# Kernel optimization log

Measured on AMD Instinct MI355X. Metric: run time of the kernel, lower is better.

Reference implementation:

```python
import jax, jax.numpy as jnp
import numpy as np

B, H, S, D = 2, 16, 2048, 128


def setup_inputs() -> dict:
    key = jax.random.key(0)
    kq, kk, kv = jax.random.split(key, 3)
    q1 = jax.random.normal(kq, (B, H, S, D), dtype=jnp.float32)
    k1 = jax.random.normal(kk, (B, H, S, D), dtype=jnp.float32)
    v1 = jax.random.normal(kv, (B, H, S, D), dtype=jnp.float32)
    scale_factor = jnp.float32(1.0 / np.sqrt(D))
    dropout_p = jnp.float32(0.5)
    return {"q1": q1, "k1": k1, "v1": v1, "scale_factor": scale_factor, "dropout_p": dropout_p}


def reference(q1, k1, v1, scale_factor, dropout_p):
    # scores: [B,H,S,S]
    qk = jnp.einsum("bhqd,bhkd->bhqk", q1, k1)
    softmax_qk = jax.nn.softmax(qk * scale_factor, axis=-1)
    # dropout (training mode, as in F.dropout default): keep w.p. 1-p, scale by 1/(1-p)
    keep = jax.random.bernoulli(jax.random.key(42), 1.0 - dropout_p, softmax_qk.shape)
    dropout_qk = jnp.where(keep, softmax_qk / (1.0 - dropout_p), 0.0)
    # output: [B,H,S,D]
    return jnp.einsum("bhqk,bhkd->bhqd", dropout_qk, v1)
```

## Files before the change

### kernel.cpp

```cpp
#include <hip/hip_runtime.h>

typedef float    f32x4  __attribute__((ext_vector_type(4)));
typedef __bf16   bf16x8 __attribute__((ext_vector_type(8)));
typedef unsigned int u32;
typedef unsigned int u32x4 __attribute__((ext_vector_type(4)));
typedef unsigned short u16;

#define S_LEN 2048
#define D_DIM 128
#define NHEAD 32
#define QBLK  64
#define KVBLK 64
#define WS_NEED (2u * NHEAD * S_LEN * D_DIM * 2u)

__device__ __forceinline__ u32 rotl32(u32 x, int r) {
  return __builtin_amdgcn_alignbit(x, x, 32 - r);
}

__device__ __forceinline__ u32 threefry_bits(u32 ctr) {
  const u32 ks1 = 42u;
  const u32 ks2 = 0x1BD11BF0u;
  u32 x0 = 0u;
  u32 x1 = ctr + ks1;
#define TFR(r) { x0 += x1; x1 = rotl32(x1, (r)); x1 ^= x0; }
  TFR(13) TFR(15) TFR(26) TFR(6)
  x0 += ks1; x1 += ks2 + 1u;
  TFR(17) TFR(29) TFR(16) TFR(24)
  x0 += ks2; x1 += 2u;
  TFR(13) TFR(15) TFR(26) TFR(6)
  x1 += ks1 + 3u;
  TFR(17) TFR(29) TFR(16) TFR(24)
  x0 += ks1; x1 += ks2 + 4u;
  TFR(13) TFR(15) TFR(26) TFR(6)
  x0 += ks2; x1 += 5u;
#undef TFR
  return x0 ^ x1;
}

__device__ __forceinline__ u16 f2bf(float f) {
  u32 u = __float_as_uint(f);
  return (u16)((u + 0x7fffu + ((u >> 16) & 1u)) >> 16);
}

__device__ __forceinline__ u32 cvtpk(float lo, float hi) {
  u32 r;
  asm("v_cvt_pk_bf16_f32 %0, %1, %2" : "=v"(r) : "v"(lo), "v"(hi));
  return r;
}

__device__ __forceinline__ float exp2a(float x) {
  float r;
  asm("v_exp_f32 %0, %1" : "=v"(r) : "v"(x));
  return r;
}

__device__ __forceinline__ void gl_lds16(const void* g, void* l) {
  __builtin_amdgcn_global_load_lds(
      (const __attribute__((address_space(1))) void*)g,
      (__attribute__((address_space(3))) void*)l, 16, 0, 0);
}

__device__ __forceinline__ u32 swzv(int d) { return (u32)((d & 7) ^ ((d >> 2) & 7)); }

__global__ void __launch_bounds__(256) prepack(
    const float* __restrict__ Kp, const float* __restrict__ Vp,
    u16* __restrict__ kimg, u16* __restrict__ vimg)
{
  __shared__ u16 vt[KVBLK * D_DIM];
  const int blk = blockIdx.x;
  const int h = blk >> 5, tk = blk & 31;
  const float* Kh = Kp + ((size_t)h * S_LEN + (size_t)tk * KVBLK) * D_DIM;
  const float* Vh = Vp + ((size_t)h * S_LEN + (size_t)tk * KVBLK) * D_DIM;
  u16* kd = kimg + (size_t)blk * (KVBLK * D_DIM);
  u16* vd = vimg + (size_t)blk * (KVBLK * D_DIM);
  const int t = threadIdx.x;

#pragma unroll
  for (int it = 0; it < 4; ++it) {
    u32 p = (u32)(it * 256 + t) * 16;
    u32 krow = p >> 8;
    u32 cb = (p & 255) ^ ((krow & 7) << 4);
    const float* src = Kh + krow * D_DIM + (cb >> 1);
    f32x4 a = *(const f32x4*)(src);
    f32x4 b = *(const f32x4*)(src + 4);
    u32x4 o;
    o.x = cvtpk(a[0], a[1]); o.y = cvtpk(a[2], a[3]);
    o.z = cvtpk(b[0], b[1]); o.w = cvtpk(b[2], b[3]);
    *(u32x4*)((char*)kd + p) = o;
  }
#pragma unroll
  for (int it = 0; it < 8; ++it) {
    int g = it * 256 + t;
    int kv = g >> 5, d4 = g & 31;
    f32x4 x = *(const f32x4*)(Vh + (size_t)kv * D_DIM + d4 * 4);
    u32* dst = (u32*)(vt + kv * D_DIM + d4 * 4);
    dst[0] = cvtpk(x[0], x[1]);
    dst[1] = cvtpk(x[2], x[3]);
  }
  __syncthreads();
#pragma unroll
  for (int it = 0; it < 4; ++it) {
    u32 p = (u32)(it * 256 + t) * 16;
    u32 vdr = p >> 7;
    u32 cb = (p & 127) ^ (swzv((int)vdr) << 4);
    u32 kv0 = cb >> 1;
    u16 e[8];
#pragma unroll
    for (int i = 0; i < 8; ++i) e[i] = vt[(kv0 + i) * D_DIM + vdr];
    u32x4 o;
    o.x = (u32)e[0] | ((u32)e[1] << 16);
    o.y = (u32)e[2] | ((u32)e[3] << 16);
    o.z = (u32)e[4] | ((u32)e[5] << 16);
    o.w = (u32)e[6] | ((u32)e[7] << 16);
    *(u32x4*)((char*)vd + p) = o;
  }
}

__global__ void __launch_bounds__(256) attn_fwd(
    const float* __restrict__ Qp, const u16* __restrict__ kimg,
    const u16* __restrict__ vimg, const float* __restrict__ scp,
    const float* __restrict__ dpp, float* __restrict__ Op)
{
  __shared__ alignas(16) u16 kbuf[KVBLK * D_DIM];
  __shared__ alignas(16) u16 vbuf[D_DIM * KVBLK];
  __shared__ alignas(16) u16 pbuf[4][16 * KVBLK];

  const int n    = blockIdx.y * gridDim.x + blockIdx.x;
  const int head = ((n & 7) << 2) | ((n >> 3) & 3);
  const int qblk = n >> 5;
  const int t  = threadIdx.x;
  const int w  = t >> 6;
  const int l  = t & 63;
  const int lg = l >> 4;
  const int lc = l & 15;

  const float scale  = scp[0];
  const float keep_p = 1.0f - dpp[0];
  const float qmul   = scale * 1.44269504088896340736f;

  u32 ithr;
  {
    float T = keep_p * 8388608.0f;
    u32 Ti = (u32)T;
    u32 thr9 = ((float)Ti == T) ? Ti : (Ti + 1u);
    ithr = (thr9 >= (1u << 23)) ? 0xFFFFFFFFu : (thr9 << 9);
  }

  const float* __restrict__ Qh = Qp + (size_t)head * (S_LEN * D_DIM);
  float*       __restrict__ Oh = Op + (size_t)head * (S_LEN * D_DIM);

  bf16x8 qf[4];
  {
    const int qrow = qblk * QBLK + w * 16 + lc;
    const float* qsrc = Qh + (size_t)qrow * D_DIM + lg * 8;
#pragma unroll
    for (int kc = 0; kc < 4; ++kc) {
      f32x4 a = *(const f32x4*)(qsrc + kc * 32);
      f32x4 b = *(const f32x4*)(qsrc + kc * 32 + 4);
      union { u32 w4[4]; bf16x8 v; } uu;
      uu.w4[0] = cvtpk(a[0] * qmul, a[1] * qmul);
      uu.w4[1] = cvtpk(a[2] * qmul, a[3] * qmul);
      uu.w4[2] = cvtpk(b[0] * qmul, b[1] * qmul);
      uu.w4[3] = cvtpk(b[2] * qmul, b[3] * qmul);
      qf[kc] = uu.v;
    }
  }

  f32x4 acc[8];
#pragma unroll
  for (int dt = 0; dt < 8; ++dt) acc[dt] = f32x4{0.f, 0.f, 0.f, 0.f};
  float lrun[4] = { 0.f, 0.f, 0.f, 0.f };

  u16* pb = &pbuf[w][0];
  const u32 qrow_c0 = (u32)(qblk * QBLK + w * 16 + lg * 4);
  const u32 ibase0  = ((u32)head * S_LEN + qrow_c0) * S_LEN;

  for (int tkv = 0; tkv < S_LEN / KVBLK; ++tkv) {
    const u16* kt  = kimg + (size_t)(head * 32 + tkv) * (KVBLK * D_DIM);
    const u16* vtg = vimg + (size_t)(head * 32 + tkv) * (KVBLK * D_DIM);
#pragma unroll
    for (int it = 0; it < 4; ++it) {
      int ck = it * 4 + w;
      gl_lds16((const char*)kt  + ck * 1024 + l * 16, (char*)kbuf + ck * 1024);
      gl_lds16((const char*)vtg + ck * 1024 + l * 16, (char*)vbuf + ck * 1024);
    }
    __syncthreads();

    f32x4 sa[4];
#pragma unroll
    for (int ct = 0; ct < 4; ++ct) sa[ct] = f32x4{0.f, 0.f, 0.f, 0.f};
#pragma unroll
    for (int kc = 0; kc < 4; ++kc) {
#pragma unroll
      for (int ct = 0; ct < 4; ++ct) {
        int krow = ct * 16 + lc;
        u32 koff = ((u32)(krow * 256 + (lg * 8 + kc * 32) * 2)) ^ ((u32)(krow & 7) << 4);
        bf16x8 kf = *(const bf16x8*)((char*)kbuf + koff);
        sa[ct] = __builtin_amdgcn_mfma_f32_16x16x32_bf16(qf[kc], kf, sa[ct], 0, 0, 0);
      }
    }

#pragma unroll
    for (int j = 0; j < 4; ++j) {
      u32 ib = ibase0 + (u32)j * S_LEN + (u32)(tkv * KVBLK) + (u32)lc;
      float p0 = exp2a(sa[0][j]);
      float p1 = exp2a(sa[1][j]);
      float p2 = exp2a(sa[2][j]);
      float p3 = exp2a(sa[3][j]);
      lrun[j] += (p0 + p1) + (p2 + p3);
      u32 b0 = threefry_bits(ib);
      u32 b1 = threefry_bits(ib + 16u);
      u32 b2 = threefry_bits(ib + 32u);
      u32 b3 = threefry_bits(ib + 48u);
      float m0 = (b0 < ithr) ? p0 : 0.0f;
      float m1 = (b1 < ithr) ? p1 : 0.0f;
      float m2 = (b2 < ithr) ? p2 : 0.0f;
      float m3 = (b3 < ithr) ? p3 : 0.0f;
      u32 pk01 = cvtpk(m0, m1);
      u32 pk23 = cvtpk(m2, m3);
      int prow = lg * 4 + j;
      u32 rb = (u32)(prow * 128 + lc * 2);
      u32 sw = (u32)(prow & 7) << 4;
      *(u16*)((char*)pb + ((rb      ) ^ sw)) = (u16)pk01;
      *(u16*)((char*)pb + ((rb +  32) ^ sw)) = (u16)(pk01 >> 16);
      *(u16*)((char*)pb + ((rb +  64) ^ sw)) = (u16)pk23;
      *(u16*)((char*)pb + ((rb +  96) ^ sw)) = (u16)(pk23 >> 16);
    }

#pragma unroll
    for (int kc2 = 0; kc2 < 2; ++kc2) {
      u32 poff = ((u32)(lc * 128 + (lg * 8 + kc2 * 32) * 2)) ^ ((u32)(lc & 7) << 4);
      bf16x8 pa = *(const bf16x8*)((char*)pb + poff);
#pragma unroll
      for (int dt = 0; dt < 8; ++dt) {
        int vd = dt * 16 + lc;
        u32 voff = ((u32)(vd * 128 + (lg * 8 + kc2 * 32) * 2)) ^ (swzv(vd) << 4);
        bf16x8 vb = *(const bf16x8*)((char*)vbuf + voff);
        acc[dt] = __builtin_amdgcn_mfma_f32_16x16x32_bf16(pa, vb, acc[dt], 0, 0, 0);
      }
    }
    __syncthreads();
  }

#pragma unroll
  for (int j = 0; j < 4; ++j) {
    float ls = lrun[j];
    ls += __shfl_xor(ls, 1, 64);
    ls += __shfl_xor(ls, 2, 64);
    ls += __shfl_xor(ls, 4, 64);
    ls += __shfl_xor(ls, 8, 64);
    float sc = (1.0f / keep_p) / ls;
    u32 qg = qrow_c0 + (u32)j;
#pragma unroll
    for (int dt = 0; dt < 8; ++dt) {
      Oh[(size_t)qg * D_DIM + dt * 16 + lc] = acc[dt][j] * sc;
    }
  }
}

__global__ void __launch_bounds__(256) attn_fwd_fb(
    const float* __restrict__ Qp, const float* __restrict__ Kp,
    const float* __restrict__ Vp, const float* __restrict__ scp,
    const float* __restrict__ dpp, float* __restrict__ Op)
{
  __shared__ alignas(16) u16 kbuf[KVBLK * D_DIM];
  __shared__ alignas(16) u16 vbuf[D_DIM * KVBLK];
  __shared__ alignas(16) u16 pbuf[4][16 * KVBLK];

  const int n    = blockIdx.y * gridDim.x + blockIdx.x;
  const int head = ((n & 7) << 2) | ((n >> 3) & 3);
  const int qblk = n >> 5;
  const int t  = threadIdx.x;
  const int w  = t >> 6;
  const int l  = t & 63;
  const int lg = l >> 4;
  const int lc = l & 15;

  const float scale  = scp[0];
  const float keep_p = 1.0f - dpp[0];
  const float qmul   = scale * 1.44269504088896340736f;
  u32 ithr;
  {
    float T = keep_p * 8388608.0f;
    u32 Ti = (u32)T;
    u32 thr9 = ((float)Ti == T) ? Ti : (Ti + 1u);
    ithr = (thr9 >= (1u << 23)) ? 0xFFFFFFFFu : (thr9 << 9);
  }

  const float* __restrict__ Qh = Qp + (size_t)head * (S_LEN * D_DIM);
  const float* __restrict__ Kh = Kp + (size_t)head * (S_LEN * D_DIM);
  const float* __restrict__ Vh = Vp + (size_t)head * (S_LEN * D_DIM);
  float*       __restrict__ Oh = Op + (size_t)head * (S_LEN * D_DIM);

  bf16x8 qf[4];
  {
    const int qrow = qblk * QBLK + w * 16 + lc;
    const float* qsrc = Qh + (size_t)qrow * D_DIM + lg * 8;
#pragma unroll
    for (int kc = 0; kc < 4; ++kc) {
      f32x4 a = *(const f32x4*)(qsrc + kc * 32);
      f32x4 b = *(const f32x4*)(qsrc + kc * 32 + 4);
      union { u16 h[8]; bf16x8 v; } uu;
#pragma unroll
      for (int i = 0; i < 4; ++i) {
        uu.h[i]     = f2bf(a[i] * qmul);
        uu.h[4 + i] = f2bf(b[i] * qmul);
      }
      qf[kc] = uu.v;
    }
  }

  f32x4 acc[8];
#pragma unroll
  for (int dt = 0; dt < 8; ++dt) acc[dt] = f32x4{0.f, 0.f, 0.f, 0.f};
  float lrun[4] = { 0.f, 0.f, 0.f, 0.f };

  u16* pb = &pbuf[w][0];
  const u32 qrow_c0 = (u32)(qblk * QBLK + w * 16 + lg * 4);
  const u32 ibase0  = ((u32)head * S_LEN + qrow_c0) * S_LEN;

  for (int tkv = 0; tkv < S_LEN / KVBLK; ++tkv) {
#pragma unroll
    for (int r = 0; r < 8; ++r) {
      int g = r * 256 + t;
      int kv = g >> 5, d4 = g & 31;
      f32x4 x = *(const f32x4*)(Kh + (size_t)(tkv * KVBLK + kv) * D_DIM + d4 * 4);
      u32 w0 = (u32)f2bf(x[0]) | ((u32)f2bf(x[1]) << 16);
      u32 w1 = (u32)f2bf(x[2]) | ((u32)f2bf(x[3]) << 16);
      u32 off = ((u32)(kv * 256 + d4 * 8)) ^ ((u32)(kv & 7) << 4);
      u32* dst = (u32*)((char*)kbuf + off);
      dst[0] = w0; dst[1] = w1;
    }
#pragma unroll
    for (int r = 0; r < 8; ++r) {
      int rowloc = w * 16 + (r & 1) * 8 + (l >> 3);
      int d4     = (r >> 1) * 8 + (l & 7);
      f32x4 x = *(const f32x4*)(Vh + (size_t)(tkv * KVBLK + rowloc) * D_DIM + d4 * 4);
      u16 mb0 = f2bf(x[0]), mb1 = f2bf(x[1]), mb2 = f2bf(x[2]), mb3 = f2bf(x[3]);
      u16 pb0 = (u16)__shfl_xor((int)mb0, 8, 64);
      u16 pb1 = (u16)__shfl_xor((int)mb1, 8, 64);
      u16 pb2 = (u16)__shfl_xor((int)mb2, 8, 64);
      u16 pb3 = (u16)__shfl_xor((int)mb3, 8, 64);
      bool ev = ((l >> 3) & 1) == 0;
      int kvp = rowloc & ~1;
      u32 wA = ev ? ((u32)mb0 | ((u32)pb0 << 16)) : ((u32)pb2 | ((u32)mb2 << 16));
      u32 wB = ev ? ((u32)mb1 | ((u32)pb1 << 16)) : ((u32)pb3 | ((u32)mb3 << 16));
      int dA = d4 * 4 + (ev ? 0 : 2);
      u32 offA = ((u32)(dA * 128 + kvp * 2)) ^ (swzv(dA) << 4);
      u32 offB = ((u32)((dA + 1) * 128 + kvp * 2)) ^ (swzv(dA + 1) << 4);
      *(u32*)((char*)vbuf + offA) = wA;
      *(u32*)((char*)vbuf + offB) = wB;
    }
    __syncthreads();

    f32x4 sa[4];
#pragma unroll
    for (int ct = 0; ct < 4; ++ct) sa[ct] = f32x4{0.f, 0.f, 0.f, 0.f};
#pragma unroll
    for (int kc = 0; kc < 4; ++kc) {
#pragma unroll
      for (int ct = 0; ct < 4; ++ct) {
        int krow = ct * 16 + lc;
        u32 koff = ((u32)(krow * 256 + (lg * 8 + kc * 32) * 2)) ^ ((u32)(krow & 7) << 4);
        bf16x8 kf = *(const bf16x8*)((char*)kbuf + koff);
        sa[ct] = __builtin_amdgcn_mfma_f32_16x16x32_bf16(qf[kc], kf, sa[ct], 0, 0, 0);
      }
    }

#pragma unroll
    for (int j = 0; j < 4; ++j) {
      u32 ib = ibase0 + (u32)j * S_LEN + (u32)(tkv * KVBLK) + (u32)lc;
      float p0 = exp2a(sa[0][j]);
      float p1 = exp2a(sa[1][j]);
      float p2 = exp2a(sa[2][j]);
      float p3 = exp2a(sa[3][j]);
      lrun[j] += (p0 + p1) + (p2 + p3);
      u32 b0 = threefry_bits(ib);
      u32 b1 = threefry_bits(ib + 16u);
      u32 b2 = threefry_bits(ib + 32u);
      u32 b3 = threefry_bits(ib + 48u);
      float m0 = (b0 < ithr) ? p0 : 0.0f;
      float m1 = (b1 < ithr) ? p1 : 0.0f;
      float m2 = (b2 < ithr) ? p2 : 0.0f;
      float m3 = (b3 < ithr) ? p3 : 0.0f;
      u32 pk01 = cvtpk(m0, m1);
      u32 pk23 = cvtpk(m2, m3);
      int prow = lg * 4 + j;
      u32 rb = (u32)(prow * 128 + lc * 2);
      u32 sw = (u32)(prow & 7) << 4;
      *(u16*)((char*)pb + ((rb      ) ^ sw)) = (u16)pk01;
      *(u16*)((char*)pb + ((rb +  32) ^ sw)) = (u16)(pk01 >> 16);
      *(u16*)((char*)pb + ((rb +  64) ^ sw)) = (u16)pk23;
      *(u16*)((char*)pb + ((rb +  96) ^ sw)) = (u16)(pk23 >> 16);
    }

#pragma unroll
    for (int kc2 = 0; kc2 < 2; ++kc2) {
      u32 poff = ((u32)(lc * 128 + (lg * 8 + kc2 * 32) * 2)) ^ ((u32)(lc & 7) << 4);
      bf16x8 pa = *(const bf16x8*)((char*)pb + poff);
#pragma unroll
      for (int dt = 0; dt < 8; ++dt) {
        int vd = dt * 16 + lc;
        u32 voff = ((u32)(vd * 128 + (lg * 8 + kc2 * 32) * 2)) ^ (swzv(vd) << 4);
        bf16x8 vb = *(const bf16x8*)((char*)vbuf + voff);
        acc[dt] = __builtin_amdgcn_mfma_f32_16x16x32_bf16(pa, vb, acc[dt], 0, 0, 0);
      }
    }
    __syncthreads();
  }

#pragma unroll
  for (int j = 0; j < 4; ++j) {
    float ls = lrun[j];
    ls += __shfl_xor(ls, 1, 64);
    ls += __shfl_xor(ls, 2, 64);
    ls += __shfl_xor(ls, 4, 64);
    ls += __shfl_xor(ls, 8, 64);
    float sc = (1.0f / keep_p) / ls;
    u32 qg = qrow_c0 + (u32)j;
#pragma unroll
    for (int dt = 0; dt < 8; ++dt) {
      Oh[(size_t)qg * D_DIM + dt * 16 + lc] = acc[dt][j] * sc;
    }
  }
}

extern "C" void kernel_launch(void* const* d_in, const int* in_sizes, int n_in,
                              void* d_out, int out_size, void* d_ws, size_t ws_size,
                              hipStream_t stream) {
  const float* q  = (const float*)d_in[0];
  const float* k  = (const float*)d_in[1];
  const float* v  = (const float*)d_in[2];
  const float* sc = (const float*)d_in[3];
  const float* dp = (const float*)d_in[4];
  float* out = (float*)d_out;
  dim3 grid(S_LEN / QBLK, NHEAD);
  dim3 block(256);
  if (ws_size >= (size_t)WS_NEED) {
    u16* kimg = (u16*)d_ws;
    u16* vimg = kimg + (size_t)NHEAD * S_LEN * D_DIM;
    hipLaunchKernelGGL(prepack, dim3(NHEAD * (S_LEN / KVBLK)), dim3(256), 0, stream, k, v, kimg, vimg);
    hipLaunchKernelGGL(attn_fwd, grid, block, 0, stream, q, kimg, vimg, sc, dp, out);
  } else {
    hipLaunchKernelGGL(attn_fwd_fb, grid, block, 0, stream, q, k, v, sc, dp, out);
  }
}
```

Measured before the change: 323.3 us.

## Grow query tile to 128 rows with 8 waves sharing each K/V tile

The main attention kernel now processes 128 query rows per block using 8 waves (512 threads) instead of 64 rows with 4 waves. Each K/V tile staged into shared memory is shared by twice as many waves, which halves the per-block global-to-LDS load traffic per query row. The grid is flattened to one dimension and the fallback kernel keeps its 64-row tiling. The trade-off is fewer, larger blocks (512 blocks) and more per-block LDS for the P buffers, which may lower occupancy or leave some tail imbalance.

```diff
diff --git a/kernel.cpp b/kernel.cpp
--- a/kernel.cpp
+++ b/kernel.cpp
@@ -9,8 +9,9 @@
 #define S_LEN 2048
 #define D_DIM 128
 #define NHEAD 32
-#define QBLK  64
+#define QBLK  128
 #define KVBLK 64
+#define NWAVE 8
 #define WS_NEED (2u * NHEAD * S_LEN * D_DIM * 2u)
 
 __device__ __forceinline__ u32 rotl32(u32 x, int r) {
@@ -116,16 +117,16 @@
   }
 }
 
-__global__ void __launch_bounds__(256) attn_fwd(
+__global__ void __launch_bounds__(512, 4) attn_fwd(
     const float* __restrict__ Qp, const u16* __restrict__ kimg,
     const u16* __restrict__ vimg, const float* __restrict__ scp,
     const float* __restrict__ dpp, float* __restrict__ Op)
 {
   __shared__ alignas(16) u16 kbuf[KVBLK * D_DIM];
   __shared__ alignas(16) u16 vbuf[D_DIM * KVBLK];
-  __shared__ alignas(16) u16 pbuf[4][16 * KVBLK];
-
-  const int n    = blockIdx.y * gridDim.x + blockIdx.x;
+  __shared__ alignas(16) u16 pbuf[NWAVE][16 * KVBLK];
+
+  const int n    = blockIdx.x;
   const int head = ((n & 7) << 2) | ((n >> 3) & 3);
   const int qblk = n >> 5;
   const int t  = threadIdx.x;
@@ -148,6 +149,8 @@
 
   const float* __restrict__ Qh = Qp + (size_t)head * (S_LEN * D_DIM);
   float*       __restrict__ Oh = Op + (size_t)head * (S_LEN * D_DIM);
+  const u16* __restrict__ kim = kimg + (size_t)head * 32 * (KVBLK * D_DIM);
+  const u16* __restrict__ vim = vimg + (size_t)head * 32 * (KVBLK * D_DIM);
 
   bf16x8 qf[4];
   {
@@ -176,13 +179,15 @@
   const u32 ibase0  = ((u32)head * S_LEN + qrow_c0) * S_LEN;
 
   for (int tkv = 0; tkv < S_LEN / KVBLK; ++tkv) {
-    const u16* kt  = kimg + (size_t)(head * 32 + tkv) * (KVBLK * D_DIM);
-    const u16* vtg = vimg + (size_t)(head * 32 + tkv) * (KVBLK * D_DIM);
-#pragma unroll
-    for (int it = 0; it < 4; ++it) {
-      int ck = it * 4 + w;
-      gl_lds16((const char*)kt  + ck * 1024 + l * 16, (char*)kbuf + ck * 1024);
-      gl_lds16((const char*)vtg + ck * 1024 + l * 16, (char*)vbuf + ck * 1024);
+    {
+      const u16* kt_ = kim + (size_t)tkv * (KVBLK * D_DIM);
+      const u16* vt_ = vim + (size_t)tkv * (KVBLK * D_DIM);
+#pragma unroll
+      for (int it = 0; it < 2; ++it) {
+        int ck = it * 8 + w;
+        gl_lds16((const char*)kt_ + ck * 1024 + l * 16, (char*)kbuf + ck * 1024);
+        gl_lds16((const char*)vt_ + ck * 1024 + l * 16, (char*)vbuf + ck * 1024);
+      }
     }
     __syncthreads();
 
@@ -294,7 +299,7 @@
 
   bf16x8 qf[4];
   {
-    const int qrow = qblk * QBLK + w * 16 + lc;
+    const int qrow = qblk * 64 + w * 16 + lc;
     const float* qsrc = Qh + (size_t)qrow * D_DIM + lg * 8;
 #pragma unroll
     for (int kc = 0; kc < 4; ++kc) {
@@ -316,7 +321,7 @@
   float lrun[4] = { 0.f, 0.f, 0.f, 0.f };
 
   u16* pb = &pbuf[w][0];
-  const u32 qrow_c0 = (u32)(qblk * QBLK + w * 16 + lg * 4);
+  const u32 qrow_c0 = (u32)(qblk * 64 + w * 16 + lg * 4);
   const u32 ibase0  = ((u32)head * S_LEN + qrow_c0) * S_LEN;
 
   for (int tkv = 0; tkv < S_LEN / KVBLK; ++tkv) {
@@ -434,14 +439,13 @@
   const float* sc = (const float*)d_in[3];
   const float* dp = (const float*)d_in[4];
   float* out = (float*)d_out;
-  dim3 grid(S_LEN / QBLK, NHEAD);
-  dim3 block(256);
   if (ws_size >= (size_t)WS_NEED) {
     u16* kimg = (u16*)d_ws;
     u16* vimg = kimg + (size_t)NHEAD * S_LEN * D_DIM;
     hipLaunchKernelGGL(prepack, dim3(NHEAD * (S_LEN / KVBLK)), dim3(256), 0, stream, k, v, kimg, vimg);
-    hipLaunchKernelGGL(attn_fwd, grid, block, 0, stream, q, kimg, vimg, sc, dp, out);
+    hipLaunchKernelGGL(attn_fwd, dim3(NHEAD * (S_LEN / QBLK)), dim3(512), 0, stream,
+                       q, kimg, vimg, sc, dp, out);
   } else {
-    hipLaunchKernelGGL(attn_fwd_fb, grid, block, 0, stream, q, k, v, sc, dp, out);
-  }
-}
+    hipLaunchKernelGGL(attn_fwd_fb, dim3(S_LEN / 64, NHEAD), dim3(256), 0, stream, q, k, v, sc, dp, out);
+  }
+}
```

After: 323.5 us. Within noise of the previous version (+0.1%).

## Load K/V fragments directly from global memory instead of staging through LDS

Applied to the files above, without the earlier changes.

The main attention kernel no longer stages K and V tiles in shared memory with global_load_lds and block-wide barriers. Each wave reads its bf16 MFMA operands straight from the prepacked global images, using swizzle offsets precomputed once, and sched_barriers replace the __syncthreads calls. This removes the LDS round trip and the block synchronisation, and frees LDS so launch bounds can ask for more resident blocks. The cost is that every wave fetches the same K/V data from global memory or cache, and the swizzled layout may not coalesce well for direct reads.

```diff
diff --git a/kernel.cpp b/kernel.cpp
--- a/kernel.cpp
+++ b/kernel.cpp
@@ -54,12 +54,6 @@
   return r;
 }
 
-__device__ __forceinline__ void gl_lds16(const void* g, void* l) {
-  __builtin_amdgcn_global_load_lds(
-      (const __attribute__((address_space(1))) void*)g,
-      (__attribute__((address_space(3))) void*)l, 16, 0, 0);
-}
-
 __device__ __forceinline__ u32 swzv(int d) { return (u32)((d & 7) ^ ((d >> 2) & 7)); }
 
 __global__ void __launch_bounds__(256) prepack(
@@ -116,13 +110,11 @@
   }
 }
 
-__global__ void __launch_bounds__(256) attn_fwd(
+__global__ void __launch_bounds__(256, 4) attn_fwd(
     const float* __restrict__ Qp, const u16* __restrict__ kimg,
     const u16* __restrict__ vimg, const float* __restrict__ scp,
     const float* __restrict__ dpp, float* __restrict__ Op)
 {
-  __shared__ alignas(16) u16 kbuf[KVBLK * D_DIM];
-  __shared__ alignas(16) u16 vbuf[D_DIM * KVBLK];
   __shared__ alignas(16) u16 pbuf[4][16 * KVBLK];
 
   const int n    = blockIdx.y * gridDim.x + blockIdx.x;
@@ -148,6 +140,8 @@
 
   const float* __restrict__ Qh = Qp + (size_t)head * (S_LEN * D_DIM);
   float*       __restrict__ Oh = Op + (size_t)head * (S_LEN * D_DIM);
+  const char* __restrict__ kim = (const char*)(kimg + (size_t)head * 32 * (KVBLK * D_DIM));
+  const char* __restrict__ vim = (const char*)(vimg + (size_t)head * 32 * (KVBLK * D_DIM));
 
   bf16x8 qf[4];
   {
@@ -166,6 +160,23 @@
     }
   }
 
+  u32 koffs[4][4];
+#pragma unroll
+  for (int kc = 0; kc < 4; ++kc)
+#pragma unroll
+    for (int ct = 0; ct < 4; ++ct) {
+      int krow = ct * 16 + lc;
+      koffs[kc][ct] = ((u32)(krow * 256 + (lg * 8 + kc * 32) * 2)) ^ ((u32)(krow & 7) << 4);
+    }
+  u32 voffs[2][8];
+#pragma unroll
+  for (int kc2 = 0; kc2 < 2; ++kc2)
+#pragma unroll
+    for (int dt = 0; dt < 8; ++dt) {
+      int vd = dt * 16 + lc;
+      voffs[kc2][dt] = ((u32)(vd * 128 + (lg * 8 + kc2 * 32) * 2)) ^ (swzv(vd) << 4);
+    }
+
   f32x4 acc[8];
 #pragma unroll
   for (int dt = 0; dt < 8; ++dt) acc[dt] = f32x4{0.f, 0.f, 0.f, 0.f};
@@ -176,15 +187,8 @@
   const u32 ibase0  = ((u32)head * S_LEN + qrow_c0) * S_LEN;
 
   for (int tkv = 0; tkv < S_LEN / KVBLK; ++tkv) {
-    const u16* kt  = kimg + (size_t)(head * 32 + tkv) * (KVBLK * D_DIM);
-    const u16* vtg = vimg + (size_t)(head * 32 + tkv) * (KVBLK * D_DIM);
-#pragma unroll
-    for (int it = 0; it < 4; ++it) {
-      int ck = it * 4 + w;
-      gl_lds16((const char*)kt  + ck * 1024 + l * 16, (char*)kbuf + ck * 1024);
-      gl_lds16((const char*)vtg + ck * 1024 + l * 16, (char*)vbuf + ck * 1024);
-    }
-    __syncthreads();
+    const char* kt = kim + (size_t)tkv * (KVBLK * D_DIM * 2);
+    const char* vt = vim + (size_t)tkv * (KVBLK * D_DIM * 2);
 
     f32x4 sa[4];
 #pragma unroll
@@ -193,9 +197,7 @@
     for (int kc = 0; kc < 4; ++kc) {
 #pragma unroll
       for (int ct = 0; ct < 4; ++ct) {
-        int krow = ct * 16 + lc;
-        u32 koff = ((u32)(krow * 256 + (lg * 8 + kc * 32) * 2)) ^ ((u32)(krow & 7) << 4);
-        bf16x8 kf = *(const bf16x8*)((char*)kbuf + koff);
+        bf16x8 kf = *(const bf16x8*)(kt + koffs[kc][ct]);
         sa[ct] = __builtin_amdgcn_mfma_f32_16x16x32_bf16(qf[kc], kf, sa[ct], 0, 0, 0);
       }
     }
@@ -227,19 +229,20 @@
       *(u16*)((char*)pb + ((rb +  96) ^ sw)) = (u16)(pk23 >> 16);
     }
 
+    __builtin_amdgcn_sched_barrier(0);
+
 #pragma unroll
     for (int kc2 = 0; kc2 < 2; ++kc2) {
       u32 poff = ((u32)(lc * 128 + (lg * 8 + kc2 * 32) * 2)) ^ ((u32)(lc & 7) << 4);
       bf16x8 pa = *(const bf16x8*)((char*)pb + poff);
 #pragma unroll
       for (int dt = 0; dt < 8; ++dt) {
-        int vd = dt * 16 + lc;
-        u32 voff = ((u32)(vd * 128 + (lg * 8 + kc2 * 32) * 2)) ^ (swzv(vd) << 4);
-        bf16x8 vb = *(const bf16x8*)((char*)vbuf + voff);
+        bf16x8 vb = *(const bf16x8*)(vt + voffs[kc2][dt]);
         acc[dt] = __builtin_amdgcn_mfma_f32_16x16x32_bf16(pa, vb, acc[dt], 0, 0, 0);
       }
     }
-    __syncthreads();
+
+    __builtin_amdgcn_sched_barrier(0);
   }
 
 #pragma unroll
@@ -294,7 +297,7 @@
 
   bf16x8 qf[4];
   {
-    const int qrow = qblk * QBLK + w * 16 + lc;
+    const int qrow = qblk * 64 + w * 16 + lc;
     const float* qsrc = Qh + (size_t)qrow * D_DIM + lg * 8;
 #pragma unroll
     for (int kc = 0; kc < 4; ++kc) {
@@ -316,7 +319,7 @@
   float lrun[4] = { 0.f, 0.f, 0.f, 0.f };
 
   u16* pb = &pbuf[w][0];
-  const u32 qrow_c0 = (u32)(qblk * QBLK + w * 16 + lg * 4);
+  const u32 qrow_c0 = (u32)(qblk * 64 + w * 16 + lg * 4);
   const u32 ibase0  = ((u32)head * S_LEN + qrow_c0) * S_LEN;
 
   for (int tkv = 0; tkv < S_LEN / KVBLK; ++tkv) {
@@ -434,14 +437,13 @@
   const float* sc = (const float*)d_in[3];
   const float* dp = (const float*)d_in[4];
   float* out = (float*)d_out;
-  dim3 grid(S_LEN / QBLK, NHEAD);
-  dim3 block(256);
   if (ws_size >= (size_t)WS_NEED) {
     u16* kimg = (u16*)d_ws;
     u16* vimg = kimg + (size_t)NHEAD * S_LEN * D_DIM;
     hipLaunchKernelGGL(prepack, dim3(NHEAD * (S_LEN / KVBLK)), dim3(256), 0, stream, k, v, kimg, vimg);
-    hipLaunchKernelGGL(attn_fwd, grid, block, 0, stream, q, kimg, vimg, sc, dp, out);
+    hipLaunchKernelGGL(attn_fwd, dim3(S_LEN / QBLK, NHEAD), dim3(256), 0, stream,
+                       q, kimg, vimg, sc, dp, out);
   } else {
-    hipLaunchKernelGGL(attn_fwd_fb, grid, block, 0, stream, q, k, v, sc, dp, out);
-  }
-}
+    hipLaunchKernelGGL(attn_fwd_fb, dim3(S_LEN / 64, NHEAD), dim3(256), 0, stream, q, k, v, sc, dp, out);
+  }
+}
```

New measurement: 487.7 us. 50.9% more time.
